# Performance work log

Hardware: AMD Instinct MI355X
Metric: run time of the kernel (lower is better)

The kernel has to match this reference:

```python
import jax, jax.numpy as jnp
import numpy as np

NUM_HEADS = 8
GROUPS = 32  # min(32, 512 // 4)
EPS = 1e-5


def group_norm(y, gamma, beta):
    B, C, L = y.shape
    yg = y.reshape(B, GROUPS, -1)  # [B, G, (C//G)*L]
    mu = yg.mean(-1, keepdims=True)
    var = yg.var(-1, keepdims=True)
    yn = ((yg - mu) * jax.lax.rsqrt(var + EPS)).reshape(B, C, L)
    return yn * gamma[:, None] + beta[:, None]


def setup_inputs() -> dict:
    key = jax.random.key(0)
    ks = jax.random.split(key, 5)
    B, C, L = 4, 512, 2048
    return {
        "x": jax.random.normal(ks[0], (B, C, L), dtype=jnp.float32),
        "Wqkv": jax.random.normal(ks[1], (3 * C, C), dtype=jnp.float32) * (C ** -0.5),
        "bqkv": jax.random.normal(ks[2], (3 * C,), dtype=jnp.float32) * 0.01,
        "Wproj": jax.random.normal(ks[3], (C, C), dtype=jnp.float32) * (C ** -0.5),
        "bproj": jax.random.normal(ks[4], (C,), dtype=jnp.float32) * 0.01,
        "gamma": jnp.ones((C,), dtype=jnp.float32),
        "beta": jnp.zeros((C,), dtype=jnp.float32),
    }


def reference(x, Wqkv, bqkv, Wproj, bproj, gamma, beta):
    B, C, L = x.shape
    H = NUM_HEADS
    D = C // H
    # 1x1 Conv1d == channel-mixing matmul
    qkv = jnp.einsum('oc,bcl->bol', Wqkv, x) + bqkv[:, None]  # [B, 3C, L]
    qkv = qkv.reshape(B, 3, H, D, L)
    q, k, v = qkv[:, 0], qkv[:, 1], qkv[:, 2]
    q = jnp.clip(q, -10.0, 10.0)
    k = jnp.clip(k, -10.0, 10.0)
    v = jnp.clip(v, -10.0, 10.0)
    scale = D ** -0.5
    attn = jnp.einsum('bhdi,bhdj->bhij', q, k) * scale  # [B, H, L, L]
    attn = jnp.clip(attn, -10.0, 10.0)
    attn = jax.nn.softmax(attn, axis=-1)
    # NaN fallback: replace whole attn with identity if any NaN (matches torch branch)
    has_nan = jnp.isnan(attn).any()
    attn = jnp.where(has_nan, jnp.eye(L, dtype=x.dtype), attn)
    out = jnp.einsum('bhij,bhdj->bhdi', attn, v)  # [B, H, D, L]
    out = out.reshape(B, C, L)
    out = jnp.einsum('oc,bcl->bol', Wproj, out) + bproj[:, None]
    return group_norm(out + x, gamma, beta)
```

## Files before the change

### kernel.cpp

```cpp
#include <hip/hip_runtime.h>
#include <cstddef>

#define B_ 4
#define C_ 512
#define L_ 2048

typedef __attribute__((ext_vector_type(8))) short  short8;
typedef __attribute__((ext_vector_type(4))) float  f32x4;
typedef __attribute__((ext_vector_type(4))) unsigned short us4;

#define AS1 __attribute__((address_space(1)))
#define AS3 __attribute__((address_space(3)))

__device__ __forceinline__ float clip10(float v){ return fminf(fmaxf(v,-10.0f),10.0f); }

__device__ __forceinline__ unsigned short f2bf(float f){
  union { float f; unsigned u; } v; v.f = f;
  unsigned r = v.u + 0x7fffu + ((v.u >> 16) & 1u);
  return (unsigned short)(r >> 16);
}
__device__ __forceinline__ unsigned pk(float lo, float hi){
  return (unsigned)f2bf(lo) | ((unsigned)f2bf(hi) << 16);
}
__device__ __forceinline__ void gl16(const void* g, void* l){
  __builtin_amdgcn_global_load_lds((const AS1 unsigned*)g, (AS3 unsigned*)l, 16, 0, 0);
}

__global__ __launch_bounds__(256) void prep_k(
    const float* __restrict__ x, const float* __restrict__ Wq,
    const float* __restrict__ Wp, unsigned short* __restrict__ xT,
    unsigned short* __restrict__ Wqb, unsigned short* __restrict__ Wpb)
{
  const int blk = blockIdx.x;
  const int t = threadIdx.x;
  if (blk < 4096){
    __shared__ float tile[32][33];
    const int b = blk>>10, rem = blk&1023;
    const int c0 = (rem>>6)*32, l0 = (rem&63)*32;
    const int cr = t>>3, lc = (t&7)*4;
    const float4 v = *(const float4*)(x + ((size_t)b*C_ + c0+cr)*L_ + l0 + lc);
    tile[cr][lc]=v.x; tile[cr][lc+1]=v.y; tile[cr][lc+2]=v.z; tile[cr][lc+3]=v.w;
    __syncthreads();
    const int lr = t>>3, cc = (t&7)*4;
    const us4 o = { f2bf(tile[cc][lr]), f2bf(tile[cc+1][lr]),
                    f2bf(tile[cc+2][lr]), f2bf(tile[cc+3][lr]) };
    *(us4*)(xT + ((size_t)b*L_ + l0+lr)*C_ + c0 + cc) = o;
  } else {
    const int i = (blk-4096)*256 + t;
    const int NQ = 1536*512/4;
    const float* src; unsigned short* dst; int j;
    if (i < NQ){ src = Wq; dst = Wqb; j = i; }
    else       { src = Wp; dst = Wpb; j = i - NQ; }
    const float4 v = *(const float4*)(src + (size_t)j*4);
    const us4 o = { f2bf(v.x), f2bf(v.y), f2bf(v.z), f2bf(v.w) };
    *(us4*)(dst + (size_t)j*4) = o;
  }
}

template<int MODE>
__global__ __launch_bounds__(256) void mfma_gemm(
    const unsigned short* __restrict__ Wb, const unsigned short* __restrict__ Bin,
    const float* __restrict__ bias,
    unsigned short* __restrict__ qT, unsigned short* __restrict__ kT,
    unsigned short* __restrict__ vN, float* __restrict__ yout)
{
  __shared__ unsigned short SA[128*64];
  __shared__ unsigned short SB[128*64];
  const int t = threadIdx.x;
  const int b = blockIdx.z;
  const int mb = blockIdx.y, n0 = blockIdx.x*128, m0 = mb*128;
  const int lane = t&63, w = t>>6, wm = w>>1, wn = w&1;
  const int n = lane&15, q4 = lane>>4;

  f32x4 acc[4][4];
#pragma unroll
  for (int i=0;i<4;i++)
#pragma unroll
    for (int j=0;j<4;j++) acc[i][j] = (f32x4){0.f,0.f,0.f,0.f};

  const unsigned short* Arow = Wb + (size_t)m0*512;
  const unsigned short* Brow = Bin + ((size_t)b*L_ + n0)*512;

  for (int kt=0; kt<8; kt++){
    const int k0 = kt*64;
    __syncthreads();
#pragma unroll
    for (int i=0;i<4;i++){
      const int ch = t + 256*i;
      const int row = ch>>3, lc = (ch&7) ^ (row&7);
      gl16(Arow + (size_t)row*512 + k0 + lc*8, &SA[ch*8]);
      gl16(Brow + (size_t)row*512 + k0 + lc*8, &SB[ch*8]);
    }
    __syncthreads();
#pragma unroll
    for (int kk=0;kk<2;kk++){
      short8 aF[4], bF[4];
      const int pc = ((kk*4+q4) ^ (n&7))*8;
#pragma unroll
      for (int mt=0;mt<4;mt++) aF[mt] = *(const short8*)&SA[(wm*64+mt*16+n)*64 + pc];
#pragma unroll
      for (int nt=0;nt<4;nt++) bF[nt] = *(const short8*)&SB[(wn*64+nt*16+n)*64 + pc];
#pragma unroll
      for (int mt=0;mt<4;mt++)
#pragma unroll
        for (int nt=0;nt<4;nt++)
          acc[mt][nt] = __builtin_amdgcn_mfma_f32_16x16x32_bf16(aF[mt], bF[nt], acc[mt][nt], 0,0,0);
    }
  }

#pragma unroll
  for (int mt=0;mt<4;mt++){
    const int obase = m0 + wm*64 + mt*16 + q4*4;
    const float b0=bias[obase], b1=bias[obase+1], b2=bias[obase+2], b3=bias[obase+3];
#pragma unroll
    for (int nt=0;nt<4;nt++){
      const int l = n0 + wn*64 + nt*16 + n;
      float r0=acc[mt][nt][0]+b0, r1=acc[mt][nt][1]+b1,
            r2=acc[mt][nt][2]+b2, r3=acc[mt][nt][3]+b3;
      if (MODE==0){
        r0=clip10(r0); r1=clip10(r1); r2=clip10(r2); r3=clip10(r3);
        const int typ = mb>>2;
        const int oin = obase - typ*512;
        if (typ < 2){
          unsigned short* dst = (typ==0) ? qT : kT;
          const us4 o = { f2bf(r0), f2bf(r1), f2bf(r2), f2bf(r3) };
          *(us4*)&dst[((size_t)b*L_ + l)*512 + oin] = o;
        } else {
          unsigned short* dst = vN + ((size_t)b*512 + oin)*L_ + l;
          dst[0]=f2bf(r0); dst[(size_t)L_]=f2bf(r1);
          dst[(size_t)2*L_]=f2bf(r2); dst[(size_t)3*L_]=f2bf(r3);
        }
      } else {
        float* dst = yout + ((size_t)b*512 + obase)*L_ + l;
        dst[0]=r0; dst[(size_t)L_]=r1; dst[(size_t)2*L_]=r2; dst[(size_t)3*L_]=r3;
      }
    }
  }
}

#define PPW 40

__global__ __launch_bounds__(256) void attn_v3(
    const unsigned short* __restrict__ qT, const unsigned short* __restrict__ kT,
    const unsigned short* __restrict__ vN, unsigned short* __restrict__ attnT)
{
  __shared__ unsigned short s_p[256*PPW];
  __shared__ unsigned short s_kv[2][2][64*64];
  const int t  = threadIdx.x;
  const int i0 = blockIdx.x*256;
  const int h  = blockIdx.y, b = blockIdx.z;
  const int lane = t&63, w = t>>6, n = lane&15, q4 = lane>>4;

  const unsigned short* kb0 = kT + (size_t)b*L_*512 + h*64;
  const unsigned short* vb  = vN + ((size_t)b*512 + h*64)*L_;

  short8 qf[4][2];
#pragma unroll
  for (int it=0; it<4; it++)
#pragma unroll
    for (int kk=0; kk<2; kk++)
      qf[it][kk] = *(const short8*)(qT + ((size_t)b*L_ + i0 + w*64 + it*16 + n)*512
                                       + h*64 + kk*32 + q4*8);

#pragma unroll
  for (int i=0;i<2;i++){
    const int ch = t + 256*i, row = ch>>3, lc = (ch&7)^(row&7);
    gl16(kb0 + (size_t)row*512 + lc*8, &s_kv[0][0][ch*8]);
    gl16(vb  + (size_t)row*L_  + lc*8, &s_kv[0][1][ch*8]);
  }

  f32x4 oacc[4][4];
  float dacc[4];
#pragma unroll
  for (int it=0;it<4;it++){ dacc[it]=0.f;
#pragma unroll
    for (int dt=0;dt<4;dt++) oacc[it][dt]=(f32x4){0.f,0.f,0.f,0.f}; }

  const float SCL = 0.125f*1.44269504089f;
  const float LIM = 14.4269504089f;
  const int   xkey = n & 6;

  int p = 0;
  for (int j0=0; j0<L_; j0+=64, p^=1){
    __syncthreads();
    if (j0+64 < L_){
#pragma unroll
      for (int i=0;i<2;i++){
        const int ch = t + 256*i, row = ch>>3, lc = (ch&7)^(row&7);
        gl16(kb0 + (size_t)(j0+64+row)*512 + lc*8,   &s_kv[p^1][0][ch*8]);
        gl16(vb  + (size_t)row*L_ + (j0+64) + lc*8,  &s_kv[p^1][1][ch*8]);
      }
    }
    const unsigned short* sk = s_kv[p][0];
    const unsigned short* sv = s_kv[p][1];

    f32x4 sacc[4][4];
#pragma unroll
    for (int it=0;it<4;it++)
#pragma unroll
      for (int jt=0;jt<4;jt++) sacc[it][jt]=(f32x4){0.f,0.f,0.f,0.f};
#pragma unroll
    for (int kk=0;kk<2;kk++){
      const int pc = ((kk*4+q4) ^ (n&7))*8;
      short8 aK[4];
#pragma unroll
      for (int jt=0;jt<4;jt++) aK[jt] = *(const short8*)&sk[(jt*16+n)*64 + pc];
#pragma unroll
      for (int it=0;it<4;it++)
#pragma unroll
        for (int jt=0;jt<4;jt++)
          sacc[it][jt] = __builtin_amdgcn_mfma_f32_16x16x32_bf16(aK[jt], qf[it][kk], sacc[it][jt], 0,0,0);
    }

#pragma unroll
    for (int half=0; half<2; half++){
#pragma unroll
      for (int it=0;it<4;it++)
#pragma unroll
        for (int jl=0;jl<2;jl++){
          const int jt = half*2 + jl;
          const float e0 = __builtin_amdgcn_exp2f(__builtin_amdgcn_fmed3f(sacc[it][jt][0]*SCL,-LIM,LIM));
          const float e1 = __builtin_amdgcn_exp2f(__builtin_amdgcn_fmed3f(sacc[it][jt][1]*SCL,-LIM,LIM));
          const float e2 = __builtin_amdgcn_exp2f(__builtin_amdgcn_fmed3f(sacc[it][jt][2]*SCL,-LIM,LIM));
          const float e3 = __builtin_amdgcn_exp2f(__builtin_amdgcn_fmed3f(sacc[it][jt][3]*SCL,-LIM,LIM));
          dacc[it] += (e0+e1)+(e2+e3);
          const unsigned long long pv =
              (unsigned long long)pk(e0,e1) | ((unsigned long long)pk(e2,e3)<<32);
          const int g = (jl*4 + q4) ^ xkey;
          *(unsigned long long*)&s_p[(w*64 + it*16 + n)*PPW + g*4] = pv;
        }
      const int pcv = ((half*4+q4) ^ (n&7))*8;
      short8 bV[4];
#pragma unroll
      for (int dt=0;dt<4;dt++) bV[dt] = *(const short8*)&sv[(dt*16+n)*64 + pcv];
      const int gr = (2*q4) ^ xkey;
#pragma unroll
      for (int it=0;it<4;it++){
        const short8 pA = *(const short8*)&s_p[(w*64 + it*16 + n)*PPW + gr*4];
#pragma unroll
        for (int dt=0;dt<4;dt++)
          oacc[it][dt] = __builtin_amdgcn_mfma_f32_16x16x32_bf16(pA, bV[dt], oacc[it][dt], 0,0,0);
      }
    }
  }

  float inv[4];
#pragma unroll
  for (int it=0;it<4;it++){
    float d = dacc[it];
    d += __shfl_xor(d, 16);
    d += __shfl_xor(d, 32);
    inv[it] = 1.0f/d;
  }
  float invr[4][4];
#pragma unroll
  for (int it=0;it<4;it++)
#pragma unroll
    for (int r=0;r<4;r++)
      invr[it][r] = __shfl(inv[it], q4*4 + r);

#pragma unroll
  for (int it=0;it<4;it++)
#pragma unroll
    for (int dt=0;dt<4;dt++)
#pragma unroll
      for (int r=0;r<4;r++){
        const size_t off = ((size_t)b*L_ + i0 + w*64 + it*16 + q4*4 + r)*512 + h*64 + dt*16 + n;
        attnT[off] = f2bf(oacc[it][dt][r]*invr[it][r]);
      }
}

__global__ __launch_bounds__(256) void gn_stats(
    const float* __restrict__ y, const float* __restrict__ x,
    float* __restrict__ part)
{
  const int blk = blockIdx.x;
  const int b = blk>>7, g = (blk>>2)&31, s = blk&3;
  const size_t base = ((size_t)b*C_ + g*16)*L_ + s*512;
  const int t = threadIdx.x;
  float sum=0.f, sq=0.f;
#pragma unroll
  for (int i=0;i<8;i++){
    const int e = i*256 + t;
    const size_t off = base + (size_t)(e>>7)*L_ + (e&127)*4;
    const float4 vy=*(const float4*)(y+off);
    const float4 vx=*(const float4*)(x+off);
    const float a=vy.x+vx.x, c=vy.y+vx.y, d=vy.z+vx.z, f=vy.w+vx.w;
    sum += (a+c)+(d+f);
    sq  += (a*a+c*c)+(d*d+f*f);
  }
  for (int off=32;off>0;off>>=1){
    sum += __shfl_down(sum,off);
    sq  += __shfl_down(sq,off);
  }
  __shared__ float red[8];
  if ((t&63)==0){ red[(t>>6)*2]=sum; red[(t>>6)*2+1]=sq; }
  __syncthreads();
  if (t==0){
    part[blk*2+0] = red[0]+red[2]+red[4]+red[6];
    part[blk*2+1] = red[1]+red[3]+red[5]+red[7];
  }
}

__global__ __launch_bounds__(256) void gn_apply(
    const float* __restrict__ y, const float* __restrict__ x,
    const float* __restrict__ part,
    const float* __restrict__ gamma, const float* __restrict__ beta,
    float* __restrict__ out)
{
  const int blk = blockIdx.x;
  const int b = blk>>7, g = (blk>>2)&31, s = blk&3;
  const int bg8 = (blk & ~3)*2;
  const float sum = (part[bg8+0]+part[bg8+2])+(part[bg8+4]+part[bg8+6]);
  const float sq  = (part[bg8+1]+part[bg8+3])+(part[bg8+5]+part[bg8+7]);
  const float mu = sum*(1.0f/32768.0f);
  const float rs = rsqrtf(sq*(1.0f/32768.0f) - mu*mu + 1e-5f);
  const size_t base = ((size_t)b*C_ + g*16)*L_ + s*512;
  const int t = threadIdx.x;
#pragma unroll
  for (int i=0;i<8;i++){
    const int e = i*256 + t;
    const int row = e>>7;
    const size_t off = base + (size_t)row*L_ + (e&127)*4;
    const int c = g*16 + row;
    const float ga = gamma[c], be = beta[c];
    const float4 vy=*(const float4*)(y+off);
    const float4 vx=*(const float4*)(x+off);
    float4 r;
    r.x=((vy.x+vx.x)-mu)*rs*ga+be;
    r.y=((vy.y+vx.y)-mu)*rs*ga+be;
    r.z=((vy.z+vx.z)-mu)*rs*ga+be;
    r.w=((vy.w+vx.w)-mu)*rs*ga+be;
    *(float4*)(out+off)=r;
  }
}

extern "C" void kernel_launch(void* const* d_in, const int* in_sizes, int n_in,
                              void* d_out, int out_size, void* d_ws, size_t ws_size,
                              hipStream_t stream)
{
  (void)in_sizes; (void)n_in; (void)out_size; (void)ws_size;
  const float* x     = (const float*)d_in[0];
  const float* Wqkv  = (const float*)d_in[1];
  const float* bqkv  = (const float*)d_in[2];
  const float* Wproj = (const float*)d_in[3];
  const float* bproj = (const float*)d_in[4];
  const float* gamma = (const float*)d_in[5];
  const float* beta  = (const float*)d_in[6];
  float* out = (float*)d_out;
  char* ws = (char*)d_ws;

  const size_t MB = 1024*1024;
  unsigned short* qT    = (unsigned short*)(ws);
  unsigned short* kT    = (unsigned short*)(ws +  8*MB);
  unsigned short* vN    = (unsigned short*)(ws + 16*MB);
  unsigned short* attnT = (unsigned short*)(ws + 24*MB);
  unsigned short* xT    = (unsigned short*)(ws + 32*MB);
  unsigned short* Wqb   = (unsigned short*)(ws + 40*MB);
  unsigned short* Wpb   = (unsigned short*)(ws + 42*MB);
  float*          y     = (float*)        (ws + 43*MB);
  float*          part  = (float*)        (ws + 59*MB);

  prep_k      <<<dim3(5120),   256,0,stream>>>(x, Wqkv, Wproj, xT, Wqb, Wpb);
  mfma_gemm<0><<<dim3(16,12,4),256,0,stream>>>(Wqb, xT,    bqkv , qT,kT,vN, nullptr);
  attn_v3     <<<dim3(8, 8, 4),256,0,stream>>>(qT, kT, vN, attnT);
  mfma_gemm<1><<<dim3(16, 4,4),256,0,stream>>>(Wpb, attnT, bproj, nullptr,nullptr,nullptr, y);
  gn_stats    <<<dim3(512),    256,0,stream>>>(y, x, part);
  gn_apply    <<<dim3(512),    256,0,stream>>>(y, x, part, gamma, beta, out);
}
```

Measured before the change: 211.1 us.

## Halve attention query tile per block to double grid size and simplify P staging

The attention kernel now gives each block 128 query rows (32 per wave) instead of 256, so the grid doubles from 256 to 512 blocks. On a GPU with many CUs, 256 blocks underfill the device, so the smaller tile aims to raise occupancy and fill the machine. The P tile is also staged as a full 64-column padded row (stride 72) written once per key tile and then read for both PV k-halves, replacing the XOR-swizzled two-half scheme. The cost is that each K/V tile is loaded from global memory twice as often overall, and there is less MFMA reuse per LDS load of K and V.

```diff
diff --git a/kernel.cpp b/kernel.cpp
--- a/kernel.cpp
+++ b/kernel.cpp
@@ -138,28 +138,28 @@
   }
 }
 
-#define PPW 40
-
-__global__ __launch_bounds__(256) void attn_v3(
+#define PP 72
+
+__global__ __launch_bounds__(256) void attn_v4(
     const unsigned short* __restrict__ qT, const unsigned short* __restrict__ kT,
     const unsigned short* __restrict__ vN, unsigned short* __restrict__ attnT)
 {
-  __shared__ unsigned short s_p[256*PPW];
+  __shared__ unsigned short s_p[128*PP];
   __shared__ unsigned short s_kv[2][2][64*64];
   const int t  = threadIdx.x;
-  const int i0 = blockIdx.x*256;
+  const int i0 = blockIdx.x*128;
   const int h  = blockIdx.y, b = blockIdx.z;
   const int lane = t&63, w = t>>6, n = lane&15, q4 = lane>>4;
 
   const unsigned short* kb0 = kT + (size_t)b*L_*512 + h*64;
   const unsigned short* vb  = vN + ((size_t)b*512 + h*64)*L_;
 
-  short8 qf[4][2];
-#pragma unroll
-  for (int it=0; it<4; it++)
+  short8 qf[2][2];
+#pragma unroll
+  for (int mt=0; mt<2; mt++)
 #pragma unroll
     for (int kk=0; kk<2; kk++)
-      qf[it][kk] = *(const short8*)(qT + ((size_t)b*L_ + i0 + w*64 + it*16 + n)*512
+      qf[mt][kk] = *(const short8*)(qT + ((size_t)b*L_ + i0 + w*32 + mt*16 + n)*512
                                        + h*64 + kk*32 + q4*8);
 
 #pragma unroll
@@ -169,16 +169,15 @@
     gl16(vb  + (size_t)row*L_  + lc*8, &s_kv[0][1][ch*8]);
   }
 
-  f32x4 oacc[4][4];
-  float dacc[4];
-#pragma unroll
-  for (int it=0;it<4;it++){ dacc[it]=0.f;
-#pragma unroll
-    for (int dt=0;dt<4;dt++) oacc[it][dt]=(f32x4){0.f,0.f,0.f,0.f}; }
+  f32x4 oacc[2][4];
+  float dacc[2];
+#pragma unroll
+  for (int mt=0;mt<2;mt++){ dacc[mt]=0.f;
+#pragma unroll
+    for (int dt=0;dt<4;dt++) oacc[mt][dt]=(f32x4){0.f,0.f,0.f,0.f}; }
 
   const float SCL = 0.125f*1.44269504089f;
   const float LIM = 14.4269504089f;
-  const int   xkey = n & 6;
 
   int p = 0;
   for (int j0=0; j0<L_; j0+=64, p^=1){
@@ -187,18 +186,18 @@
 #pragma unroll
       for (int i=0;i<2;i++){
         const int ch = t + 256*i, row = ch>>3, lc = (ch&7)^(row&7);
-        gl16(kb0 + (size_t)(j0+64+row)*512 + lc*8,   &s_kv[p^1][0][ch*8]);
-        gl16(vb  + (size_t)row*L_ + (j0+64) + lc*8,  &s_kv[p^1][1][ch*8]);
+        gl16(kb0 + (size_t)(j0+64+row)*512 + lc*8,  &s_kv[p^1][0][ch*8]);
+        gl16(vb  + (size_t)row*L_ + (j0+64) + lc*8, &s_kv[p^1][1][ch*8]);
       }
     }
     const unsigned short* sk = s_kv[p][0];
     const unsigned short* sv = s_kv[p][1];
 
-    f32x4 sacc[4][4];
-#pragma unroll
-    for (int it=0;it<4;it++)
-#pragma unroll
-      for (int jt=0;jt<4;jt++) sacc[it][jt]=(f32x4){0.f,0.f,0.f,0.f};
+    f32x4 sacc[2][4];
+#pragma unroll
+    for (int mt=0;mt<2;mt++)
+#pragma unroll
+      for (int jt=0;jt<4;jt++) sacc[mt][jt]=(f32x4){0.f,0.f,0.f,0.f};
 #pragma unroll
     for (int kk=0;kk<2;kk++){
       const int pc = ((kk*4+q4) ^ (n&7))*8;
@@ -206,67 +205,66 @@
 #pragma unroll
       for (int jt=0;jt<4;jt++) aK[jt] = *(const short8*)&sk[(jt*16+n)*64 + pc];
 #pragma unroll
-      for (int it=0;it<4;it++)
+      for (int mt=0;mt<2;mt++)
 #pragma unroll
         for (int jt=0;jt<4;jt++)
-          sacc[it][jt] = __builtin_amdgcn_mfma_f32_16x16x32_bf16(aK[jt], qf[it][kk], sacc[it][jt], 0,0,0);
-    }
-
-#pragma unroll
-    for (int half=0; half<2; half++){
-#pragma unroll
-      for (int it=0;it<4;it++)
-#pragma unroll
-        for (int jl=0;jl<2;jl++){
-          const int jt = half*2 + jl;
-          const float e0 = __builtin_amdgcn_exp2f(__builtin_amdgcn_fmed3f(sacc[it][jt][0]*SCL,-LIM,LIM));
-          const float e1 = __builtin_amdgcn_exp2f(__builtin_amdgcn_fmed3f(sacc[it][jt][1]*SCL,-LIM,LIM));
-          const float e2 = __builtin_amdgcn_exp2f(__builtin_amdgcn_fmed3f(sacc[it][jt][2]*SCL,-LIM,LIM));
-          const float e3 = __builtin_amdgcn_exp2f(__builtin_amdgcn_fmed3f(sacc[it][jt][3]*SCL,-LIM,LIM));
-          dacc[it] += (e0+e1)+(e2+e3);
-          const unsigned long long pv =
-              (unsigned long long)pk(e0,e1) | ((unsigned long long)pk(e2,e3)<<32);
-          const int g = (jl*4 + q4) ^ xkey;
-          *(unsigned long long*)&s_p[(w*64 + it*16 + n)*PPW + g*4] = pv;
-        }
-      const int pcv = ((half*4+q4) ^ (n&7))*8;
-      short8 bV[4];
+          sacc[mt][jt] = __builtin_amdgcn_mfma_f32_16x16x32_bf16(aK[jt], qf[mt][kk], sacc[mt][jt], 0,0,0);
+    }
+
+#pragma unroll
+    for (int mt=0;mt<2;mt++)
+#pragma unroll
+      for (int jt=0;jt<4;jt++){
+        const float e0 = __builtin_amdgcn_exp2f(__builtin_amdgcn_fmed3f(sacc[mt][jt][0]*SCL,-LIM,LIM));
+        const float e1 = __builtin_amdgcn_exp2f(__builtin_amdgcn_fmed3f(sacc[mt][jt][1]*SCL,-LIM,LIM));
+        const float e2 = __builtin_amdgcn_exp2f(__builtin_amdgcn_fmed3f(sacc[mt][jt][2]*SCL,-LIM,LIM));
+        const float e3 = __builtin_amdgcn_exp2f(__builtin_amdgcn_fmed3f(sacc[mt][jt][3]*SCL,-LIM,LIM));
+        dacc[mt] += (e0+e1)+(e2+e3);
+        const unsigned long long pv =
+            (unsigned long long)pk(e0,e1) | ((unsigned long long)pk(e2,e3)<<32);
+        *(unsigned long long*)&s_p[(w*32 + mt*16 + n)*PP + jt*16 + q4*4] = pv;
+      }
+
+#pragma unroll
+    for (int kk=0;kk<2;kk++){
+      const int pcv = ((kk*4+q4) ^ (n&7))*8;
+      short8 bV[4], pA[2];
 #pragma unroll
       for (int dt=0;dt<4;dt++) bV[dt] = *(const short8*)&sv[(dt*16+n)*64 + pcv];
-      const int gr = (2*q4) ^ xkey;
-#pragma unroll
-      for (int it=0;it<4;it++){
-        const short8 pA = *(const short8*)&s_p[(w*64 + it*16 + n)*PPW + gr*4];
+#pragma unroll
+      for (int mt=0;mt<2;mt++)
+        pA[mt] = *(const short8*)&s_p[(w*32 + mt*16 + n)*PP + kk*32 + q4*8];
+#pragma unroll
+      for (int mt=0;mt<2;mt++)
 #pragma unroll
         for (int dt=0;dt<4;dt++)
-          oacc[it][dt] = __builtin_amdgcn_mfma_f32_16x16x32_bf16(pA, bV[dt], oacc[it][dt], 0,0,0);
-      }
-    }
-  }
-
-  float inv[4];
-#pragma unroll
-  for (int it=0;it<4;it++){
-    float d = dacc[it];
+          oacc[mt][dt] = __builtin_amdgcn_mfma_f32_16x16x32_bf16(pA[mt], bV[dt], oacc[mt][dt], 0,0,0);
+    }
+  }
+
+  float inv[2];
+#pragma unroll
+  for (int mt=0;mt<2;mt++){
+    float d = dacc[mt];
     d += __shfl_xor(d, 16);
     d += __shfl_xor(d, 32);
-    inv[it] = 1.0f/d;
-  }
-  float invr[4][4];
-#pragma unroll
-  for (int it=0;it<4;it++)
+    inv[mt] = 1.0f/d;
+  }
+  float invr[2][4];
+#pragma unroll
+  for (int mt=0;mt<2;mt++)
 #pragma unroll
     for (int r=0;r<4;r++)
-      invr[it][r] = __shfl(inv[it], q4*4 + r);
-
-#pragma unroll
-  for (int it=0;it<4;it++)
+      invr[mt][r] = __shfl(inv[mt], q4*4 + r);
+
+#pragma unroll
+  for (int mt=0;mt<2;mt++)
 #pragma unroll
     for (int dt=0;dt<4;dt++)
 #pragma unroll
       for (int r=0;r<4;r++){
-        const size_t off = ((size_t)b*L_ + i0 + w*64 + it*16 + q4*4 + r)*512 + h*64 + dt*16 + n;
-        attnT[off] = f2bf(oacc[it][dt][r]*invr[it][r]);
+        const size_t off = ((size_t)b*L_ + i0 + w*32 + mt*16 + q4*4 + r)*512 + h*64 + dt*16 + n;
+        attnT[off] = f2bf(oacc[mt][dt][r]*invr[mt][r]);
       }
 }
 
@@ -363,7 +361,7 @@
 
   prep_k      <<<dim3(5120),   256,0,stream>>>(x, Wqkv, Wproj, xT, Wqb, Wpb);
   mfma_gemm<0><<<dim3(16,12,4),256,0,stream>>>(Wqb, xT,    bqkv , qT,kT,vN, nullptr);
-  attn_v3     <<<dim3(8, 8, 4),256,0,stream>>>(qT, kT, vN, attnT);
+  attn_v4     <<<dim3(16,8,4), 256,0,stream>>>(qT, kT, vN, attnT);
   mfma_gemm<1><<<dim3(16, 4,4),256,0,stream>>>(Wpb, attnT, bproj, nullptr,nullptr,nullptr, y);
   gn_stats    <<<dim3(512),    256,0,stream>>>(y, x, part);
   gn_apply    <<<dim3(512),    256,0,stream>>>(y, x, part, gamma, beta, out);
```

New measurement: 201.3 us. -4.6%, faster.
